# Performance work log

Hardware: AMD Instinct MI355X
Metric: run time of the kernel (lower is better)

## Reference

```python
import jax, jax.numpy as jnp
import numpy as np
from jax import lax

FEAT_STRIDE = 16
BOX_SIZES = (4.0, 8.0, 12.0, 16.0, 24.0, 32.0, 48.0, 64.0, 96.0)
SCALE = 1.0
NUM_ANCHORS = 9
MIN_SIZE = 3.0          # rpn_config.MIN_SIZE (feature-map units)
NMS_THRESH = 0.7        # rpn_config.NMS_THRESH
PRE_NMS_TOP_N = 6000    # rpn_config.PRE_NMS_TOP_N
POST_NMS_TOP_N = 300    # rpn_config.POST_NMS_TOP_N


def _generate_anchors(H, W):
    # [A,H,W,4] boxes in (x, y, w, h); coord 0 pairs with the height axis,
    # matching clip_boxes_batch which clips index 0/2 against `length`=height.
    s = jnp.asarray(BOX_SIZES, jnp.float32) * SCALE                  # [A]
    cy = jnp.arange(H, dtype=jnp.float32) + 0.5
    cx = jnp.arange(W, dtype=jnp.float32) + 0.5
    shp = (NUM_ANCHORS, H, W)
    x0 = jnp.broadcast_to(cy[None, :, None] - s[:, None, None] / 2, shp)
    y0 = jnp.broadcast_to(cx[None, None, :] - s[:, None, None] / 2, shp)
    wh = jnp.broadcast_to(s[:, None, None], shp)
    return jnp.stack([x0, y0, wh, wh], axis=-1)


def _clip_boxes(boxes, H, W):
    # Faithful to clip_boxes_batch: clamp all entries at 0, convert to corners,
    # clamp x against height, y against width, convert back to (x,y,w,h).
    b = jnp.maximum(boxes, 0.0)
    x1, y1, w, h = b[..., 0], b[..., 1], b[..., 2], b[..., 3]
    x2, y2 = x1 + w, y1 + h
    x1 = jnp.minimum(x1, H)
    y1 = jnp.minimum(y1, W)
    x2 = jnp.minimum(x2, H)
    y2 = jnp.minimum(y2, W)
    return jnp.stack([x1, y1, x2 - x1, y2 - y1], axis=-1)


def setup_inputs() -> dict:
    key = jax.random.key(0)
    k1, k2 = jax.random.split(key)
    scores = jax.random.uniform(k1, (1, NUM_ANCHORS, 128, 128), dtype=jnp.float32)
    bbox_deltas = jax.random.normal(k2, (1, 4 * NUM_ANCHORS, 128, 128), dtype=jnp.float32)
    image_metadata = jnp.zeros((1, 3), dtype=jnp.float32)  # unused by forward
    return {"scores": scores, "bbox_deltas": bbox_deltas, "image_metadata": image_metadata}


def reference(scores, bbox_deltas, image_metadata):
    b, A, H, W = scores.shape
    anchors = _generate_anchors(H, W)[None]                 # [1,A,H,W,4]
    # torch view chain (A*4,H,W)->(A,4,H,W)->(A,H,W,4) over contiguous memory
    # is a single reshape of the flat buffer:
    deltas = bbox_deltas.reshape(b, A, H, W, 4)
    boxes = _clip_boxes(anchors + deltas, float(H), float(W))
    flat = boxes.reshape(-1, 4)                             # [N,4], N=A*H*W
    keep = (flat[:, 2] >= MIN_SIZE) & (flat[:, 3] >= MIN_SIZE)
    sc = jnp.where(keep, scores.reshape(-1), -jnp.inf)      # mask instead of compaction (jit-safe)
    _, top = lax.top_k(sc, PRE_NMS_TOP_N)                   # score-descending pre-NMS top-N
    props = flat[top]                                       # [K,4]

    # --- greedy NMS, processing order = descending y2 (as in source `nms`) ---
    x1, y1, w, h = props[:, 0], props[:, 1], props[:, 2], props[:, 3]
    x2, y2 = x1 + w, y1 + h
    order = jnp.argsort(-y2)
    x1, y1, x2, y2 = x1[order], y1[order], x2[order], y2[order]
    area = jnp.maximum((x2 - x1) * (y2 - y1), 1e-6)         # areas = l*b in source
    iw = jnp.maximum(jnp.minimum(x2[:, None], x2[None, :]) - jnp.maximum(x1[:, None], x1[None, :]) + 1.0, 0.0)
    ih = jnp.maximum(jnp.minimum(y2[:, None], y2[None, :]) - jnp.maximum(y1[:, None], y1[None, :]) + 1.0, 0.0)
    ov = iw * ih / area[None, :]                            # intersection / area[j], as in source

    K = PRE_NMS_TOP_N

    def body(valid, i):
        supp = (ov[i] >= NMS_THRESH) & valid
        supp = supp.at[i].set(False)
        return jnp.where(valid[i], valid & ~supp, valid), None

    valid, _ = lax.scan(body, jnp.ones((K,), bool), jnp.arange(K))

    # kept boxes first, in processing order; pad with zeros to POST_NMS_TOP_N
    perm = jnp.argsort(jnp.where(valid, jnp.arange(K), K))
    sel = perm[:POST_NMS_TOP_N]
    out = props[order][sel] * valid[sel][:, None].astype(props.dtype)
    return out[None]                                        # [1, POST_NMS_TOP_N, 4]
```

## Files before the change

kernel.cpp:

```cpp
#include <hip/hip_runtime.h>
#include <cstdint>
#include <cstddef>

#define N_TOT   147456
#define K_PRE   6000
#define K_POST  300
#define CAP     32768
#define MW      188
#define ROWS_PAD 6144
#define CH      256
#define NCH     24
#define CT      128
#define ROWB    24
#define COLB    47
#define NTILE   (ROWB*COLB)
#define G       16
#define NBLK    576
#define HBLK    144
#define NGRP    24
#define GSZ     24

#define OFF_CAND 0u
#define OFF_P    262144u
#define OFF_YK   358144u
#define OFF_OP   406272u
#define OFF_Q    502272u
#define OFF_BND  598272u
#define OFF_MASK 622336u

__constant__ float c_sizes[9] = {4.f,8.f,12.f,16.f,24.f,32.f,48.f,64.f,96.f};

__device__ uint32_t g_hist[4096];
__device__ uint32_t g_cnt;
__device__ uint32_t g_barL[8][NGRP * 16];
__device__ uint32_t g_barR[8 * 16];
__device__ uint32_t g_rel[8][NGRP * 16];

__device__ __forceinline__ void astore32(uint32_t* p, uint32_t v) {
    __hip_atomic_store(p, v, __ATOMIC_RELAXED, __HIP_MEMORY_SCOPE_AGENT);
}
__device__ __forceinline__ void astore64(uint64_t* p, uint64_t v) {
    __hip_atomic_store(p, v, __ATOMIC_RELAXED, __HIP_MEMORY_SCOPE_AGENT);
}
__device__ __forceinline__ void astoreF4(float4* p, float4 v) {
    union { float4 f; uint64_t u[2]; } c; c.f = v;
    astore64((uint64_t*)p, c.u[0]);
    astore64(((uint64_t*)p) + 1, c.u[1]);
}

__device__ __forceinline__ void flagBarrier(int i) {
    __syncthreads();
    if (threadIdx.x == 0) {
        int grp = (int)(blockIdx.x / GSZ);
        int mem = (int)(blockIdx.x % GSZ);
        uint32_t t = __hip_atomic_fetch_add(&g_barL[i][grp * 16], 1u,
                          __ATOMIC_RELAXED, __HIP_MEMORY_SCOPE_AGENT);
        uint32_t round = t / GSZ;
        if ((t % GSZ) == GSZ - 1u)
            __hip_atomic_fetch_add(&g_barR[i * 16], 1u,
                __ATOMIC_RELAXED, __HIP_MEMORY_SCOPE_AGENT);
        uint32_t tries = 0;
        if (mem == 0) {
            uint32_t target = (round + 1u) * NGRP;
            while (__hip_atomic_load(&g_barR[i * 16], __ATOMIC_RELAXED,
                                     __HIP_MEMORY_SCOPE_AGENT) < target) {
                __builtin_amdgcn_s_sleep(4);
                if (++tries > (1u << 20)) break;
            }
            astore32(&g_rel[i][grp * 16], round + 1u);
        } else {
            while (__hip_atomic_load(&g_rel[i][grp * 16], __ATOMIC_RELAXED,
                                     __HIP_MEMORY_SCOPE_AGENT) < round + 1u) {
                __builtin_amdgcn_s_sleep(4);
                if (++tries > (1u << 20)) break;
            }
        }
        asm volatile("" ::: "memory");
    }
    __syncthreads();
}

__device__ __forceinline__ void compute_box(int idx, const float* __restrict__ deltas,
                                            float& px1, float& py1, float& pw, float& ph) {
    int a   = idx >> 14;
    int rem = idx & 16383;
    int h   = rem >> 7;
    int w   = rem & 127;
    float s    = c_sizes[a];
    float half = s * 0.5f;
    const float4 d = *(const float4*)(deltas + (size_t)a * 65536 + (size_t)rem * 4);
    float b0 = (((float)h + 0.5f) - half) + d.x;
    float b1 = (((float)w + 0.5f) - half) + d.y;
    float b2 = s + d.z;
    float b3 = s + d.w;
    b0 = fmaxf(b0, 0.0f); b1 = fmaxf(b1, 0.0f);
    b2 = fmaxf(b2, 0.0f); b3 = fmaxf(b3, 0.0f);
    float x1 = b0, y1 = b1;
    float x2 = b0 + b2, y2 = b1 + b3;
    x1 = fminf(x1, 128.0f); y1 = fminf(y1, 128.0f);
    x2 = fminf(x2, 128.0f); y2 = fminf(y2, 128.0f);
    px1 = x1; py1 = y1; pw = x2 - x1; ph = y2 - y1;
}

__device__ __forceinline__ uint32_t waveReduceSum(uint32_t v) {
    #pragma unroll
    for (int o = 32; o > 0; o >>= 1) v += __shfl_xor(v, o, 64);
    return v;
}

__global__ void __launch_bounds__(256, 4) mega(const float* __restrict__ scores,
                                               const float* __restrict__ deltas,
                                               float* __restrict__ out,
                                               char* __restrict__ ws) {
    __shared__ __align__(16) char smem[17664];

    uint64_t* cand = (uint64_t*)(ws + OFF_CAND);
    float4*   P    = (float4*)(ws + OFF_P);
    uint64_t* yk   = (uint64_t*)(ws + OFF_YK);
    float4*   OP   = (float4*)(ws + OFF_OP);
    float4*   Q    = (float4*)(ws + OFF_Q);
    float*    Bnd  = (float*)(ws + OFF_BND);
    uint32_t* mask = (uint32_t*)(ws + OFF_MASK);

    const int tid  = threadIdx.x;
    const int bid  = blockIdx.x;
    const int wave = tid >> 6, lane = tid & 63;

    uint32_t k4x = 0, k4y = 0, k4z = 0, k4w = 0;

    if (bid < HBLK) {
        uint32_t* lh = (uint32_t*)smem;
        for (int i = tid; i < 4096; i += 256) lh[i] = 0u;
        __syncthreads();
        int t4 = (bid * 256 + tid) * 4;
        float4 sc4 = *(const float4*)(scores + t4);
        uint32_t k4[4];
        #pragma unroll
        for (int e = 0; e < 4; e++) {
            int idx = t4 + e;
            float px1, py1, pw, ph;
            compute_box(idx, deltas, px1, py1, pw, ph);
            bool keep = (pw >= 3.0f) && (ph >= 3.0f);
            float sc = (&sc4.x)[e];
            uint32_t key = keep ? __float_as_uint(sc) : 0u;
            k4[e] = key;
            atomicAdd(&lh[key >> 20], 1u);
        }
        k4x = k4[0]; k4y = k4[1]; k4z = k4[2]; k4w = k4[3];
        __syncthreads();
        for (int i = tid; i < 4096; i += 256) {
            uint32_t v = lh[i];
            if (v) atomicAdd(&g_hist[i], v);
        }
    }
    flagBarrier(0);

    if (bid < HBLK) {
        uint32_t* lh   = (uint32_t*)smem;
        uint32_t* seg  = (uint32_t*)(smem + 16384);
        uint32_t* bshp = (uint32_t*)(smem + 16384 + 1024);
        uint32_t* lcnt = bshp + 1;
        uint32_t* lbas = bshp + 2;
        if (tid == 0) lcnt[0] = 0u;
        for (int i = tid; i < 4096; i += 256) lh[i] = g_hist[i];
        __syncthreads();
        uint32_t s = 0;
        #pragma unroll
        for (int q = 0; q < 16; q++) s += lh[tid * 16 + q];
        seg[tid] = s;
        __syncthreads();
        for (int off = 1; off < 256; off <<= 1) {
            uint32_t v = seg[tid];
            if (tid + off < 256) v += seg[tid + off];
            __syncthreads();
            seg[tid] = v;
            __syncthreads();
        }
        uint32_t St  = seg[tid];
        uint32_t St1 = (tid < 255) ? seg[tid + 1] : 0u;
        if (St >= K_PRE && St1 < K_PRE) {
            uint32_t c2 = St1;
            uint32_t bstar = 0u;
            for (int q = 15; q >= 0; q--) {
                c2 += lh[tid * 16 + q];
                if (c2 >= K_PRE) { bstar = (uint32_t)(tid * 16 + q); break; }
            }
            bshp[0] = bstar;
        }
        if (tid == 0 && seg[0] < K_PRE) bshp[0] = 0u;
        __syncthreads();
        uint32_t bstar = bshp[0];
        int t4 = (bid * 256 + tid) * 4;
        bool s0 = (k4x >> 20) >= bstar;
        bool s1 = (k4y >> 20) >= bstar;
        bool s2 = (k4z >> 20) >= bstar;
        bool s3 = (k4w >> 20) >= bstar;
        uint32_t nsel = (uint32_t)s0 + s1 + s2 + s3;
        uint32_t myoff = 0u;
        if (nsel) myoff = atomicAdd(lcnt, nsel);
        __syncthreads();
        if (tid == 0) lbas[0] = atomicAdd(&g_cnt, lcnt[0]);
        __syncthreads();
        uint32_t pos = lbas[0] + myoff;
        if (s0) { if (pos < CAP) astore64(&cand[pos], ((uint64_t)k4x << 32) | (uint32_t)(~(uint32_t)(t4 + 0))); pos++; }
        if (s1) { if (pos < CAP) astore64(&cand[pos], ((uint64_t)k4y << 32) | (uint32_t)(~(uint32_t)(t4 + 1))); pos++; }
        if (s2) { if (pos < CAP) astore64(&cand[pos], ((uint64_t)k4z << 32) | (uint32_t)(~(uint32_t)(t4 + 2))); pos++; }
        if (s3) { if (pos < CAP) astore64(&cand[pos], ((uint64_t)k4w << 32) | (uint32_t)(~(uint32_t)(t4 + 3))); }
    }
    flagBarrier(1);

    {
        uint32_t (*part)[G] = (uint32_t (*)[G])smem;
        uint32_t C = g_cnt;
        if (C > CAP) C = CAP;
        uint32_t nGroups = (C + G - 1) / G;
        for (uint32_t g = bid; g < nGroups; g += NBLK) {
            uint32_t b = g * G;
            uint64_t m[G];
            uint32_t cnt[G];
            #pragma unroll
            for (int q = 0; q < G; q++) {
                m[q] = (b + q < C) ? cand[b + q] : ~0ull;
                cnt[q] = 0u;
            }
            for (uint32_t j0 = 0; j0 < C; j0 += 1024) {
                uint32_t ja = j0 + tid, jb = ja + 256, jc = ja + 512, jd = ja + 768;
                uint64_t ka = (ja < C) ? cand[ja] : 0ull;
                uint64_t kb = (jb < C) ? cand[jb] : 0ull;
                uint64_t kc = (jc < C) ? cand[jc] : 0ull;
                uint64_t kd = (jd < C) ? cand[jd] : 0ull;
                #pragma unroll
                for (int q = 0; q < G; q++)
                    cnt[q] += (uint32_t)(ka > m[q]) + (uint32_t)(kb > m[q])
                            + (uint32_t)(kc > m[q]) + (uint32_t)(kd > m[q]);
            }
            #pragma unroll
            for (int q = 0; q < G; q++) cnt[q] = waveReduceSum(cnt[q]);
            if (lane == 0) {
                #pragma unroll
                for (int q = 0; q < G; q++) part[wave][q] = cnt[q];
            }
            __syncthreads();
            if (tid < G && b + tid < C) {
                uint32_t r = part[0][tid] + part[1][tid] + part[2][tid] + part[3][tid];
                if (r < K_PRE) {
                    int idx = (int)(~((uint32_t)cand[b + tid]));
                    float px1, py1, pw, ph;
                    compute_box(idx, deltas, px1, py1, pw, ph);
                    astoreF4(&P[r], make_float4(px1, py1, pw, ph));
                    float y2 = py1 + ph;
                    astore64(&yk[r], ((uint64_t)__float_as_uint(y2) << 32) | (uint32_t)(~r));
                }
            }
            __syncthreads();
        }
    }
    flagBarrier(2);

    if (bid < K_PRE / G) {
        uint32_t (*part)[G] = (uint32_t (*)[G])smem;
        uint32_t b = (uint32_t)bid * G;
        uint64_t m[G];
        uint32_t cnt[G];
        #pragma unroll
        for (int q = 0; q < G; q++) {
            m[q] = yk[b + q];
            cnt[q] = 0u;
        }
        for (uint32_t j0 = 0; j0 < K_PRE; j0 += 1024) {
            uint32_t ja = j0 + tid, jb = ja + 256, jc = ja + 512, jd = ja + 768;
            uint64_t ka = (ja < K_PRE) ? yk[ja] : 0ull;
            uint64_t kb = (jb < K_PRE) ? yk[jb] : 0ull;
            uint64_t kc = (jc < K_PRE) ? yk[jc] : 0ull;
            uint64_t kd = (jd < K_PRE) ? yk[jd] : 0ull;
            #pragma unroll
            for (int q = 0; q < G; q++)
                cnt[q] += (uint32_t)(ka > m[q]) + (uint32_t)(kb > m[q])
                        + (uint32_t)(kc > m[q]) + (uint32_t)(kd > m[q]);
        }
        #pragma unroll
        for (int q = 0; q < G; q++) cnt[q] = waveReduceSum(cnt[q]);
        if (lane == 0) {
            #pragma unroll
            for (int q = 0; q < G; q++) part[wave][q] = cnt[q];
        }
        __syncthreads();
        if (tid < G) {
            uint32_t r = part[0][tid] + part[1][tid] + part[2][tid] + part[3][tid];
            float4 p = P[b + tid];
            astoreF4(&OP[r], p);
            float x1 = p.x, y1 = p.y;
            float x2 = x1 + p.z, y2 = y1 + p.w;
            float area = fmaxf((x2 - x1) * (y2 - y1), 1e-6f);
            astoreF4(&Q[r], make_float4(x1, y1, x2, y2));
            const double Mc = (double)0.7f - 0x1.0p-25;
            double c = Mc * (double)area;
            float Bf = (float)c;
            if (!((double)Bf > c)) Bf = __int_as_float(__float_as_int(Bf) + 1);
            astore32((uint32_t*)&Bnd[r], __float_as_uint(Bf));
        }
    }
    flagBarrier(3);

    {
        float4* qs = (float4*)smem;
        float*  bs = (float*)(smem + CT * 16);
        for (uint32_t t = bid; t < NTILE; t += NBLK) {
            int bx = (int)(t % ROWB);
            int by = (int)(t / ROWB);
            int i  = bx * 256 + tid;
            int c0 = by * CT;
            int ncols = min(CT, K_PRE - c0);
            bool rowok = (i < K_PRE);
            float4 qi = rowok ? Q[i] : make_float4(0.f, 0.f, 0.f, 0.f);
            __syncthreads();
            for (int j = tid; j < ncols; j += 256) {
                qs[j] = Q[c0 + j];
                bs[j] = Bnd[c0 + j];
            }
            __syncthreads();
            uint32_t bw[4];
            #pragma unroll
            for (int w = 0; w < 4; w++) {
                uint32_t bits = 0u;
                int jb = w * 32;
                int jn = min(32, ncols - jb);
                #pragma unroll 8
                for (int b = 0; b < jn; b++) {
                    int j = jb + b;
                    float4 qj = qs[j];
                    float iw = fminf(qi.z, qj.z) - fmaxf(qi.x, qj.x) + 1.0f;
                    iw = fmaxf(iw, 0.0f);
                    float ih = fminf(qi.w, qj.w) - fmaxf(qi.y, qj.y) + 1.0f;
                    ih = fmaxf(ih, 0.0f);
                    float d = iw * ih;
                    bits |= (d >= bs[j]) ? (1u << b) : 0u;
                }
                int gj = c0 + jb;
                uint32_t selfo = (uint32_t)(i - gj);
                if (selfo < 32u) bits &= ~(1u << selfo);
                bw[w] = bits;
            }
            if (rowok) {
                uint64_t* bp = (uint64_t*)&mask[(size_t)i * MW + (c0 >> 5)];
                astore64(bp,     ((uint64_t)bw[1] << 32) | bw[0]);
                astore64(bp + 1, ((uint64_t)bw[3] << 32) | bw[2]);
            }
        }
    }
    flagBarrier(4);
    if (bid != 0) return;

    {
        uint32_t* rem  = (uint32_t*)smem;
        uint32_t* sidx = rem + 192;
        uint32_t* svL  = sidx + CH;
        uint32_t* pref = svL + 192;
        uint32_t* nsSh = pref + MW;
        if (tid < 16) {
            #pragma unroll
            for (int q = 0; q < 16; q++) g_hist[tid * 16 + q] = 0u;
        }
        if (tid == 16) g_cnt = 0u;
        if (tid < 192) { rem[tid] = 0u; svL[tid] = 0u; }
        for (int i = tid; i < K_POST * 4; i += 256) out[i] = 0.0f;
        __syncthreads();
        uint4 s00 = make_uint4(0,0,0,0), s01 = s00, s10 = s00, s11 = s00;
        uint4 s20 = s00, s21 = s00, s30 = s00, s31 = s00;
        if (tid < 64) {
            const uint32_t* p0 = mask + (size_t)(tid) * MW;
            s00 = *(const uint4*)p0;       s01 = *(const uint4*)(p0 + 4);
            const uint32_t* p1 = mask + (size_t)(64 + tid) * MW;
            s10 = *(const uint4*)p1;       s11 = *(const uint4*)(p1 + 4);
            const uint32_t* p2 = mask + (size_t)(128 + tid) * MW;
            s20 = *(const uint4*)p2;       s21 = *(const uint4*)(p2 + 4);
            const uint32_t* p3 = mask + (size_t)(192 + tid) * MW;
            s30 = *(const uint4*)p3;       s31 = *(const uint4*)(p3 + 4);
        }
        for (int c = 0; c < NCH; c++) {
            int base = c * CH;
            if (tid < 64) {
                uint64_t w0 = ~(((uint64_t)rem[8*c+1] << 32) | (uint64_t)rem[8*c+0]);
                uint64_t w1 = ~(((uint64_t)rem[8*c+3] << 32) | (uint64_t)rem[8*c+2]);
                uint64_t w2 = ~(((uint64_t)rem[8*c+5] << 32) | (uint64_t)rem[8*c+4]);
                uint64_t w3 = ~(((uint64_t)rem[8*c+7] << 32) | (uint64_t)rem[8*c+6]);
                int rows = K_PRE - base;
                if (rows < CH) {
                    auto msk = [](int v) -> uint64_t {
                        return v <= 0 ? 0ull : (v >= 64 ? ~0ull : ((1ull << v) - 1ull));
                    };
                    w0 &= msk(rows); w1 &= msk(rows - 64);
                    w2 &= msk(rows - 128); w3 &= msk(rows - 192);
                }
                uint64_t sv0 = 0ull, sv1 = 0ull, sv2 = 0ull, sv3 = 0ull;
                while (w0 | w1 | w2 | w3) {
                    int k;
                    uint32_t a0, a1, a2, a3, a4, a5, a6, a7;
                    if (w0) {
                        k = __ffsll((unsigned long long)w0) - 1;
                        sv0 |= 1ull << k; w0 &= ~(1ull << k);
                        a0 = (uint32_t)__builtin_amdgcn_readlane((int)s00.x, k);
                        a1 = (uint32_t)__builtin_amdgcn_readlane((int)s00.y, k);
                        a2 = (uint32_t)__builtin_amdgcn_readlane((int)s00.z, k);
                        a3 = (uint32_t)__builtin_amdgcn_readlane((int)s00.w, k);
                        a4 = (uint32_t)__builtin_amdgcn_readlane((int)s01.x, k);
                        a5 = (uint32_t)__builtin_amdgcn_readlane((int)s01.y, k);
                        a6 = (uint32_t)__builtin_amdgcn_readlane((int)s01.z, k);
                        a7 = (uint32_t)__builtin_amdgcn_readlane((int)s01.w, k);
                    } else if (w1) {
                        k = __ffsll((unsigned long long)w1) - 1;
                        sv1 |= 1ull << k; w1 &= ~(1ull << k);
                        a0 = (uint32_t)__builtin_amdgcn_readlane((int)s10.x, k);
                        a1 = (uint32_t)__builtin_amdgcn_readlane((int)s10.y, k);
                        a2 = (uint32_t)__builtin_amdgcn_readlane((int)s10.z, k);
                        a3 = (uint32_t)__builtin_amdgcn_readlane((int)s10.w, k);
                        a4 = (uint32_t)__builtin_amdgcn_readlane((int)s11.x, k);
                        a5 = (uint32_t)__builtin_amdgcn_readlane((int)s11.y, k);
                        a6 = (uint32_t)__builtin_amdgcn_readlane((int)s11.z, k);
                        a7 = (uint32_t)__builtin_amdgcn_readlane((int)s11.w, k);
                    } else if (w2) {
                        k = __ffsll((unsigned long long)w2) - 1;
                        sv2 |= 1ull << k; w2 &= ~(1ull << k);
                        a0 = (uint32_t)__builtin_amdgcn_readlane((int)s20.x, k);
                        a1 = (uint32_t)__builtin_amdgcn_readlane((int)s20.y, k);
                        a2 = (uint32_t)__builtin_amdgcn_readlane((int)s20.z, k);
                        a3 = (uint32_t)__builtin_amdgcn_readlane((int)s20.w, k);
                        a4 = (uint32_t)__builtin_amdgcn_readlane((int)s21.x, k);
                        a5 = (uint32_t)__builtin_amdgcn_readlane((int)s21.y, k);
                        a6 = (uint32_t)__builtin_amdgcn_readlane((int)s21.z, k);
                        a7 = (uint32_t)__builtin_amdgcn_readlane((int)s21.w, k);
                    } else {
                        k = __ffsll((unsigned long long)w3) - 1;
                        sv3 |= 1ull << k; w3 &= ~(1ull << k);
                        a0 = (uint32_t)__builtin_amdgcn_readlane((int)s30.x, k);
                        a1 = (uint32_t)__builtin_amdgcn_readlane((int)s30.y, k);
                        a2 = (uint32_t)__builtin_amdgcn_readlane((int)s30.z, k);
                        a3 = (uint32_t)__builtin_amdgcn_readlane((int)s30.w, k);
                        a4 = (uint32_t)__builtin_amdgcn_readlane((int)s31.x, k);
                        a5 = (uint32_t)__builtin_amdgcn_readlane((int)s31.y, k);
                        a6 = (uint32_t)__builtin_amdgcn_readlane((int)s31.z, k);
                        a7 = (uint32_t)__builtin_amdgcn_readlane((int)s31.w, k);
                    }
                    w0 &= ~(((uint64_t)a1 << 32) | (uint64_t)a0);
                    w1 &= ~(((uint64_t)a3 << 32) | (uint64_t)a2);
                    w2 &= ~(((uint64_t)a5 << 32) | (uint64_t)a4);
                    w3 &= ~(((uint64_t)a7 << 32) | (uint64_t)a6);
                }
                uint32_t n0 = (uint32_t)__popcll(sv0), n1 = (uint32_t)__popcll(sv1);
                uint32_t n2 = (uint32_t)__popcll(sv2), n3 = (uint32_t)__popcll(sv3);
                uint32_t o1 = n0, o2 = n0 + n1, o3 = n0 + n1 + n2, ns = o3 + n3;
                if (tid == 0) {
                    svL[8*c+0] = (uint32_t)sv0; svL[8*c+1] = (uint32_t)(sv0 >> 32);
                    svL[8*c+2] = (uint32_t)sv1; svL[8*c+3] = (uint32_t)(sv1 >> 32);
                    svL[8*c+4] = (uint32_t)sv2; svL[8*c+5] = (uint32_t)(sv2 >> 32);
                    svL[8*c+6] = (uint32_t)sv3; svL[8*c+7] = (uint32_t)(sv3 >> 32);
                    nsSh[0] = ns;
                }
                uint64_t lowm = (1ull << tid) - 1ull;
                if ((sv0 >> tid) & 1ull) sidx[      __popcll(sv0 & lowm)] = (uint32_t)(base + tid);
                if ((sv1 >> tid) & 1ull) sidx[o1 +  __popcll(sv1 & lowm)] = (uint32_t)(base + 64 + tid);
                if ((sv2 >> tid) & 1ull) sidx[o2 +  __popcll(sv2 & lowm)] = (uint32_t)(base + 128 + tid);
                if ((sv3 >> tid) & 1ull) sidx[o3 +  __popcll(sv3 & lowm)] = (uint32_t)(base + 192 + tid);
                if (ns) {
                    uint32_t nsPad = (ns + 31u) & ~31u;
                    uint32_t first;
                    if      (sv0) first = (uint32_t)base +       (uint32_t)(__ffsll((unsigned long long)sv0) - 1);
                    else if (sv1) first = (uint32_t)base + 64u + (uint32_t)(__ffsll((unsigned long long)sv1) - 1);
                    else if (sv2) first = (uint32_t)base + 128u+ (uint32_t)(__ffsll((unsigned long long)sv2) - 1);
                    else          first = (uint32_t)base + 192u+ (uint32_t)(__ffsll((unsigned long long)sv3) - 1);
                    #pragma unroll
                    for (int rr = 0; rr < 4; rr++) {
                        uint32_t ii = (uint32_t)tid + 64u * rr;
                        if (ii >= ns && ii < nsPad) sidx[ii] = first;
                    }
                }
                if (c + 1 < NCH) {
                    const uint32_t* p0 = mask + (size_t)(base + 256 + tid) * MW + 8*(c+1);
                    s00 = *(const uint4*)p0;  s01 = *(const uint4*)(p0 + 4);
                    const uint32_t* p1 = p0 + (size_t)64 * MW;
                    s10 = *(const uint4*)p1;  s11 = *(const uint4*)(p1 + 4);
                    const uint32_t* p2 = p1 + (size_t)64 * MW;
                    s20 = *(const uint4*)p2;  s21 = *(const uint4*)(p2 + 4);
                    const uint32_t* p3 = p2 + (size_t)64 * MW;
                    s30 = *(const uint4*)p3;  s31 = *(const uint4*)(p3 + 4);
                }
            }
            __syncthreads();
            int w = tid - 64;
            if (w >= 0 && w < MW) {
                uint32_t nsPad = (nsSh[0] + 31u) & ~31u;
                uint32_t acc = rem[w];
                for (uint32_t t2 = 0; t2 < nsPad; t2 += 32) {
                    uint32_t r[32];
                    #pragma unroll
                    for (int q = 0; q < 32; q++)
                        r[q] = mask[(size_t)sidx[t2 + q] * MW + w];
                    uint32_t o = 0u;
                    #pragma unroll
                    for (int q = 0; q < 32; q++) o |= r[q];
                    acc |= o;
                }
                rem[w] = acc;
            }
            __syncthreads();
        }
        if (tid < MW) {
            uint32_t vv = svL[tid] & ~rem[tid];
            if (tid == MW - 1) vv &= 0xFFFFu;
            rem[tid] = vv;
        }
        __syncthreads();
        if (tid == 0) {
            uint32_t run = 0;
            for (int w2 = 0; w2 < MW; w2++) { pref[w2] = run; run += (uint32_t)__popc(rem[w2]); }
        }
        __syncthreads();
        if (tid < MW) {
            uint32_t b = rem[tid];
            uint32_t r = pref[tid];
            int basebit = tid * 32;
            while (b && r < K_POST) {
                int bit = __ffs(b) - 1;
                b &= b - 1u;
                float4 pp = OP[basebit + bit];
                *(float4*)(out + (size_t)r * 4) = pp;
                r++;
            }
        }
    }
}

extern "C" void kernel_launch(void* const* d_in, const int* in_sizes, int n_in,
                              void* d_out, int out_size, void* d_ws, size_t ws_size,
                              hipStream_t stream) {
    (void)in_sizes; (void)n_in; (void)out_size; (void)ws_size;
    const float* scores = (const float*)d_in[0];
    const float* deltas = (const float*)d_in[1];
    float* out = (float*)d_out;
    char* ws = (char*)d_ws;
    mega<<<NBLK, 256, 0, stream>>>(scores, deltas, out, ws);
}
```

Measured before the change: 159.4 us.

## Split final NMS scan into separate kernel and scope first barrier to histogram blocks

The last grid barrier is replaced by a kernel boundary: the mask-building kernel ends and a separate single-block kernel runs the greedy NMS scan and output compaction. The first barrier now synchronizes only the 144 histogram blocks, so the other blocks skip it. The barrier sleep interval is halved, and some atomic stores become plain stores now that kernel-boundary ordering applies. This trades one spin barrier across all blocks for an extra launch gap.

New measurement: 154.9 us. 1.03x faster.

```diff
diff --git a/kernel.cpp b/kernel.cpp
--- a/kernel.cpp
+++ b/kernel.cpp
@@ -17,7 +17,6 @@
 #define G       16
 #define NBLK    576
 #define HBLK    144
-#define NGRP    24
 #define GSZ     24
 
 #define OFF_CAND 0u
@@ -32,9 +31,9 @@
 
 __device__ uint32_t g_hist[4096];
 __device__ uint32_t g_cnt;
-__device__ uint32_t g_barL[8][NGRP * 16];
-__device__ uint32_t g_barR[8 * 16];
-__device__ uint32_t g_rel[8][NGRP * 16];
+__device__ uint32_t g_barL[4][GSZ * 16];
+__device__ uint32_t g_barR[4 * 16];
+__device__ uint32_t g_rel[4][GSZ * 16];
 
 __device__ __forceinline__ void astore32(uint32_t* p, uint32_t v) {
     __hip_atomic_store(p, v, __ATOMIC_RELAXED, __HIP_MEMORY_SCOPE_AGENT);
@@ -48,11 +47,12 @@
     astore64(((uint64_t*)p) + 1, c.u[1]);
 }
 
-__device__ __forceinline__ void flagBarrier(int i) {
+__device__ __forceinline__ void treeBarrier(int i, int nprt) {
     __syncthreads();
     if (threadIdx.x == 0) {
-        int grp = (int)(blockIdx.x / GSZ);
-        int mem = (int)(blockIdx.x % GSZ);
+        int ngrp = nprt / GSZ;
+        int grp  = (int)(blockIdx.x / GSZ);
+        int mem  = (int)(blockIdx.x % GSZ);
         uint32_t t = __hip_atomic_fetch_add(&g_barL[i][grp * 16], 1u,
                           __ATOMIC_RELAXED, __HIP_MEMORY_SCOPE_AGENT);
         uint32_t round = t / GSZ;
@@ -61,17 +61,17 @@
                 __ATOMIC_RELAXED, __HIP_MEMORY_SCOPE_AGENT);
         uint32_t tries = 0;
         if (mem == 0) {
-            uint32_t target = (round + 1u) * NGRP;
+            uint32_t target = (round + 1u) * (uint32_t)ngrp;
             while (__hip_atomic_load(&g_barR[i * 16], __ATOMIC_RELAXED,
                                      __HIP_MEMORY_SCOPE_AGENT) < target) {
-                __builtin_amdgcn_s_sleep(4);
+                __builtin_amdgcn_s_sleep(2);
                 if (++tries > (1u << 20)) break;
             }
             astore32(&g_rel[i][grp * 16], round + 1u);
         } else {
             while (__hip_atomic_load(&g_rel[i][grp * 16], __ATOMIC_RELAXED,
                                      __HIP_MEMORY_SCOPE_AGENT) < round + 1u) {
-                __builtin_amdgcn_s_sleep(4);
+                __builtin_amdgcn_s_sleep(2);
                 if (++tries > (1u << 20)) break;
             }
         }
@@ -108,10 +108,9 @@
     return v;
 }
 
-__global__ void __launch_bounds__(256, 4) mega(const float* __restrict__ scores,
-                                               const float* __restrict__ deltas,
-                                               float* __restrict__ out,
-                                               char* __restrict__ ws) {
+__global__ void __launch_bounds__(256, 4) fusedA(const float* __restrict__ scores,
+                                                 const float* __restrict__ deltas,
+                                                 char* __restrict__ ws) {
     __shared__ __align__(16) char smem[17664];
 
     uint64_t* cand = (uint64_t*)(ws + OFF_CAND);
@@ -126,88 +125,88 @@
     const int bid  = blockIdx.x;
     const int wave = tid >> 6, lane = tid & 63;
 
-    uint32_t k4x = 0, k4y = 0, k4z = 0, k4w = 0;
-
     if (bid < HBLK) {
-        uint32_t* lh = (uint32_t*)smem;
-        for (int i = tid; i < 4096; i += 256) lh[i] = 0u;
-        __syncthreads();
-        int t4 = (bid * 256 + tid) * 4;
-        float4 sc4 = *(const float4*)(scores + t4);
-        uint32_t k4[4];
-        #pragma unroll
-        for (int e = 0; e < 4; e++) {
-            int idx = t4 + e;
-            float px1, py1, pw, ph;
-            compute_box(idx, deltas, px1, py1, pw, ph);
-            bool keep = (pw >= 3.0f) && (ph >= 3.0f);
-            float sc = (&sc4.x)[e];
-            uint32_t key = keep ? __float_as_uint(sc) : 0u;
-            k4[e] = key;
-            atomicAdd(&lh[key >> 20], 1u);
-        }
-        k4x = k4[0]; k4y = k4[1]; k4z = k4[2]; k4w = k4[3];
-        __syncthreads();
-        for (int i = tid; i < 4096; i += 256) {
-            uint32_t v = lh[i];
-            if (v) atomicAdd(&g_hist[i], v);
-        }
-    }
-    flagBarrier(0);
-
-    if (bid < HBLK) {
-        uint32_t* lh   = (uint32_t*)smem;
-        uint32_t* seg  = (uint32_t*)(smem + 16384);
-        uint32_t* bshp = (uint32_t*)(smem + 16384 + 1024);
-        uint32_t* lcnt = bshp + 1;
-        uint32_t* lbas = bshp + 2;
-        if (tid == 0) lcnt[0] = 0u;
-        for (int i = tid; i < 4096; i += 256) lh[i] = g_hist[i];
-        __syncthreads();
-        uint32_t s = 0;
-        #pragma unroll
-        for (int q = 0; q < 16; q++) s += lh[tid * 16 + q];
-        seg[tid] = s;
-        __syncthreads();
-        for (int off = 1; off < 256; off <<= 1) {
-            uint32_t v = seg[tid];
-            if (tid + off < 256) v += seg[tid + off];
-            __syncthreads();
-            seg[tid] = v;
-            __syncthreads();
-        }
-        uint32_t St  = seg[tid];
-        uint32_t St1 = (tid < 255) ? seg[tid + 1] : 0u;
-        if (St >= K_PRE && St1 < K_PRE) {
-            uint32_t c2 = St1;
-            uint32_t bstar = 0u;
-            for (int q = 15; q >= 0; q--) {
-                c2 += lh[tid * 16 + q];
-                if (c2 >= K_PRE) { bstar = (uint32_t)(tid * 16 + q); break; }
-            }
-            bshp[0] = bstar;
-        }
-        if (tid == 0 && seg[0] < K_PRE) bshp[0] = 0u;
-        __syncthreads();
-        uint32_t bstar = bshp[0];
-        int t4 = (bid * 256 + tid) * 4;
-        bool s0 = (k4x >> 20) >= bstar;
-        bool s1 = (k4y >> 20) >= bstar;
-        bool s2 = (k4z >> 20) >= bstar;
-        bool s3 = (k4w >> 20) >= bstar;
-        uint32_t nsel = (uint32_t)s0 + s1 + s2 + s3;
-        uint32_t myoff = 0u;
-        if (nsel) myoff = atomicAdd(lcnt, nsel);
-        __syncthreads();
-        if (tid == 0) lbas[0] = atomicAdd(&g_cnt, lcnt[0]);
-        __syncthreads();
-        uint32_t pos = lbas[0] + myoff;
-        if (s0) { if (pos < CAP) astore64(&cand[pos], ((uint64_t)k4x << 32) | (uint32_t)(~(uint32_t)(t4 + 0))); pos++; }
-        if (s1) { if (pos < CAP) astore64(&cand[pos], ((uint64_t)k4y << 32) | (uint32_t)(~(uint32_t)(t4 + 1))); pos++; }
-        if (s2) { if (pos < CAP) astore64(&cand[pos], ((uint64_t)k4z << 32) | (uint32_t)(~(uint32_t)(t4 + 2))); pos++; }
-        if (s3) { if (pos < CAP) astore64(&cand[pos], ((uint64_t)k4w << 32) | (uint32_t)(~(uint32_t)(t4 + 3))); }
-    }
-    flagBarrier(1);
+        uint32_t k4x, k4y, k4z, k4w;
+        {
+            uint32_t* lh = (uint32_t*)smem;
+            for (int i = tid; i < 4096; i += 256) lh[i] = 0u;
+            __syncthreads();
+            int t4 = (bid * 256 + tid) * 4;
+            float4 sc4 = *(const float4*)(scores + t4);
+            uint32_t k4[4];
+            #pragma unroll
+            for (int e = 0; e < 4; e++) {
+                int idx = t4 + e;
+                float px1, py1, pw, ph;
+                compute_box(idx, deltas, px1, py1, pw, ph);
+                bool keep = (pw >= 3.0f) && (ph >= 3.0f);
+                float sc = (&sc4.x)[e];
+                uint32_t key = keep ? __float_as_uint(sc) : 0u;
+                k4[e] = key;
+                atomicAdd(&lh[key >> 20], 1u);
+            }
+            k4x = k4[0]; k4y = k4[1]; k4z = k4[2]; k4w = k4[3];
+            __syncthreads();
+            for (int i = tid; i < 4096; i += 256) {
+                uint32_t v = lh[i];
+                if (v) atomicAdd(&g_hist[i], v);
+            }
+        }
+        treeBarrier(0, HBLK);
+        {
+            uint32_t* lh   = (uint32_t*)smem;
+            uint32_t* seg  = (uint32_t*)(smem + 16384);
+            uint32_t* bshp = (uint32_t*)(smem + 16384 + 1024);
+            uint32_t* lcnt = bshp + 1;
+            uint32_t* lbas = bshp + 2;
+            if (tid == 0) lcnt[0] = 0u;
+            for (int i = tid; i < 4096; i += 256) lh[i] = g_hist[i];
+            __syncthreads();
+            uint32_t s = 0;
+            #pragma unroll
+            for (int q = 0; q < 16; q++) s += lh[tid * 16 + q];
+            seg[tid] = s;
+            __syncthreads();
+            for (int off = 1; off < 256; off <<= 1) {
+                uint32_t v = seg[tid];
+                if (tid + off < 256) v += seg[tid + off];
+                __syncthreads();
+                seg[tid] = v;
+                __syncthreads();
+            }
+            uint32_t St  = seg[tid];
+            uint32_t St1 = (tid < 255) ? seg[tid + 1] : 0u;
+            if (St >= K_PRE && St1 < K_PRE) {
+                uint32_t c2 = St1;
+                uint32_t bstar = 0u;
+                for (int q = 15; q >= 0; q--) {
+                    c2 += lh[tid * 16 + q];
+                    if (c2 >= K_PRE) { bstar = (uint32_t)(tid * 16 + q); break; }
+                }
+                bshp[0] = bstar;
+            }
+            if (tid == 0 && seg[0] < K_PRE) bshp[0] = 0u;
+            __syncthreads();
+            uint32_t bstar = bshp[0];
+            int t4 = (bid * 256 + tid) * 4;
+            bool s0 = (k4x >> 20) >= bstar;
+            bool s1 = (k4y >> 20) >= bstar;
+            bool s2 = (k4z >> 20) >= bstar;
+            bool s3 = (k4w >> 20) >= bstar;
+            uint32_t nsel = (uint32_t)s0 + s1 + s2 + s3;
+            uint32_t myoff = 0u;
+            if (nsel) myoff = atomicAdd(lcnt, nsel);
+            __syncthreads();
+            if (tid == 0) lbas[0] = atomicAdd(&g_cnt, lcnt[0]);
+            __syncthreads();
+            uint32_t pos = lbas[0] + myoff;
+            if (s0) { if (pos < CAP) astore64(&cand[pos], ((uint64_t)k4x << 32) | (uint32_t)(~(uint32_t)(t4 + 0))); pos++; }
+            if (s1) { if (pos < CAP) astore64(&cand[pos], ((uint64_t)k4y << 32) | (uint32_t)(~(uint32_t)(t4 + 1))); pos++; }
+            if (s2) { if (pos < CAP) astore64(&cand[pos], ((uint64_t)k4z << 32) | (uint32_t)(~(uint32_t)(t4 + 2))); pos++; }
+            if (s3) { if (pos < CAP) astore64(&cand[pos], ((uint64_t)k4w << 32) | (uint32_t)(~(uint32_t)(t4 + 3))); }
+        }
+    }
+    treeBarrier(1, NBLK);
 
     {
         uint32_t (*part)[G] = (uint32_t (*)[G])smem;
@@ -255,7 +254,7 @@
             __syncthreads();
         }
     }
-    flagBarrier(2);
+    treeBarrier(2, NBLK);
 
     if (bid < K_PRE / G) {
         uint32_t (*part)[G] = (uint32_t (*)[G])smem;
@@ -288,7 +287,7 @@
         if (tid < G) {
             uint32_t r = part[0][tid] + part[1][tid] + part[2][tid] + part[3][tid];
             float4 p = P[b + tid];
-            astoreF4(&OP[r], p);
+            OP[r] = p;
             float x1 = p.x, y1 = p.y;
             float x2 = x1 + p.z, y2 = y1 + p.w;
             float area = fmaxf((x2 - x1) * (y2 - y1), 1e-6f);
@@ -300,7 +299,7 @@
             astore32((uint32_t*)&Bnd[r], __float_as_uint(Bf));
         }
     }
-    flagBarrier(3);
+    treeBarrier(3, NBLK);
 
     {
         float4* qs = (float4*)smem;
@@ -342,190 +341,190 @@
                 bw[w] = bits;
             }
             if (rowok) {
-                uint64_t* bp = (uint64_t*)&mask[(size_t)i * MW + (c0 >> 5)];
-                astore64(bp,     ((uint64_t)bw[1] << 32) | bw[0]);
-                astore64(bp + 1, ((uint64_t)bw[3] << 32) | bw[2]);
-            }
-        }
-    }
-    flagBarrier(4);
-    if (bid != 0) return;
-
-    {
-        uint32_t* rem  = (uint32_t*)smem;
-        uint32_t* sidx = rem + 192;
-        uint32_t* svL  = sidx + CH;
-        uint32_t* pref = svL + 192;
-        uint32_t* nsSh = pref + MW;
-        if (tid < 16) {
-            #pragma unroll
-            for (int q = 0; q < 16; q++) g_hist[tid * 16 + q] = 0u;
-        }
-        if (tid == 16) g_cnt = 0u;
-        if (tid < 192) { rem[tid] = 0u; svL[tid] = 0u; }
-        for (int i = tid; i < K_POST * 4; i += 256) out[i] = 0.0f;
+                *(uint4*)&mask[(size_t)i * MW + (c0 >> 5)] =
+                    make_uint4(bw[0], bw[1], bw[2], bw[3]);
+            }
+        }
+    }
+}
+
+__global__ void __launch_bounds__(256) k_scan(const uint32_t* __restrict__ mask,
+                                              const float4* __restrict__ OP,
+                                              float* __restrict__ out) {
+    __shared__ uint32_t rem[192];
+    __shared__ uint32_t sidx[CH];
+    __shared__ uint32_t svL[192];
+    __shared__ uint32_t nsSh;
+    __shared__ uint32_t pref[MW];
+    int tid = threadIdx.x;
+    if (tid < 16) {
+        #pragma unroll
+        for (int q = 0; q < 16; q++) g_hist[tid * 16 + q] = 0u;
+    }
+    if (tid == 16) g_cnt = 0u;
+    if (tid < 192) { rem[tid] = 0u; svL[tid] = 0u; }
+    for (int i = tid; i < K_POST * 4; i += 256) out[i] = 0.0f;
+    __syncthreads();
+    uint4 s00 = make_uint4(0,0,0,0), s01 = s00, s10 = s00, s11 = s00;
+    uint4 s20 = s00, s21 = s00, s30 = s00, s31 = s00;
+    if (tid < 64) {
+        const uint32_t* p0 = mask + (size_t)(tid) * MW;
+        s00 = *(const uint4*)p0;       s01 = *(const uint4*)(p0 + 4);
+        const uint32_t* p1 = mask + (size_t)(64 + tid) * MW;
+        s10 = *(const uint4*)p1;       s11 = *(const uint4*)(p1 + 4);
+        const uint32_t* p2 = mask + (size_t)(128 + tid) * MW;
+        s20 = *(const uint4*)p2;       s21 = *(const uint4*)(p2 + 4);
+        const uint32_t* p3 = mask + (size_t)(192 + tid) * MW;
+        s30 = *(const uint4*)p3;       s31 = *(const uint4*)(p3 + 4);
+    }
+    for (int c = 0; c < NCH; c++) {
+        int base = c * CH;
+        if (tid < 64) {
+            uint64_t w0 = ~(((uint64_t)rem[8*c+1] << 32) | (uint64_t)rem[8*c+0]);
+            uint64_t w1 = ~(((uint64_t)rem[8*c+3] << 32) | (uint64_t)rem[8*c+2]);
+            uint64_t w2 = ~(((uint64_t)rem[8*c+5] << 32) | (uint64_t)rem[8*c+4]);
+            uint64_t w3 = ~(((uint64_t)rem[8*c+7] << 32) | (uint64_t)rem[8*c+6]);
+            int rows = K_PRE - base;
+            if (rows < CH) {
+                auto msk = [](int v) -> uint64_t {
+                    return v <= 0 ? 0ull : (v >= 64 ? ~0ull : ((1ull << v) - 1ull));
+                };
+                w0 &= msk(rows); w1 &= msk(rows - 64);
+                w2 &= msk(rows - 128); w3 &= msk(rows - 192);
+            }
+            uint64_t sv0 = 0ull, sv1 = 0ull, sv2 = 0ull, sv3 = 0ull;
+            while (w0 | w1 | w2 | w3) {
+                int k;
+                uint32_t a0, a1, a2, a3, a4, a5, a6, a7;
+                if (w0) {
+                    k = __ffsll((unsigned long long)w0) - 1;
+                    sv0 |= 1ull << k; w0 &= ~(1ull << k);
+                    a0 = (uint32_t)__builtin_amdgcn_readlane((int)s00.x, k);
+                    a1 = (uint32_t)__builtin_amdgcn_readlane((int)s00.y, k);
+                    a2 = (uint32_t)__builtin_amdgcn_readlane((int)s00.z, k);
+                    a3 = (uint32_t)__builtin_amdgcn_readlane((int)s00.w, k);
+                    a4 = (uint32_t)__builtin_amdgcn_readlane((int)s01.x, k);
+                    a5 = (uint32_t)__builtin_amdgcn_readlane((int)s01.y, k);
+                    a6 = (uint32_t)__builtin_amdgcn_readlane((int)s01.z, k);
+                    a7 = (uint32_t)__builtin_amdgcn_readlane((int)s01.w, k);
+                } else if (w1) {
+                    k = __ffsll((unsigned long long)w1) - 1;
+                    sv1 |= 1ull << k; w1 &= ~(1ull << k);
+                    a0 = (uint32_t)__builtin_amdgcn_readlane((int)s10.x, k);
+                    a1 = (uint32_t)__builtin_amdgcn_readlane((int)s10.y, k);
+                    a2 = (uint32_t)__builtin_amdgcn_readlane((int)s10.z, k);
+                    a3 = (uint32_t)__builtin_amdgcn_readlane((int)s10.w, k);
+                    a4 = (uint32_t)__builtin_amdgcn_readlane((int)s11.x, k);
+                    a5 = (uint32_t)__builtin_amdgcn_readlane((int)s11.y, k);
+                    a6 = (uint32_t)__builtin_amdgcn_readlane((int)s11.z, k);
+                    a7 = (uint32_t)__builtin_amdgcn_readlane((int)s11.w, k);
+                } else if (w2) {
+                    k = __ffsll((unsigned long long)w2) - 1;
+                    sv2 |= 1ull << k; w2 &= ~(1ull << k);
+                    a0 = (uint32_t)__builtin_amdgcn_readlane((int)s20.x, k);
+                    a1 = (uint32_t)__builtin_amdgcn_readlane((int)s20.y, k);
+                    a2 = (uint32_t)__builtin_amdgcn_readlane((int)s20.z, k);
+                    a3 = (uint32_t)__builtin_amdgcn_readlane((int)s20.w, k);
+                    a4 = (uint32_t)__builtin_amdgcn_readlane((int)s21.x, k);
+                    a5 = (uint32_t)__builtin_amdgcn_readlane((int)s21.y, k);
+                    a6 = (uint32_t)__builtin_amdgcn_readlane((int)s21.z, k);
+                    a7 = (uint32_t)__builtin_amdgcn_readlane((int)s21.w, k);
+                } else {
+                    k = __ffsll((unsigned long long)w3) - 1;
+                    sv3 |= 1ull << k; w3 &= ~(1ull << k);
+                    a0 = (uint32_t)__builtin_amdgcn_readlane((int)s30.x, k);
+                    a1 = (uint32_t)__builtin_amdgcn_readlane((int)s30.y, k);
+                    a2 = (uint32_t)__builtin_amdgcn_readlane((int)s30.z, k);
+                    a3 = (uint32_t)__builtin_amdgcn_readlane((int)s30.w, k);
+                    a4 = (uint32_t)__builtin_amdgcn_readlane((int)s31.x, k);
+                    a5 = (uint32_t)__builtin_amdgcn_readlane((int)s31.y, k);
+                    a6 = (uint32_t)__builtin_amdgcn_readlane((int)s31.z, k);
+                    a7 = (uint32_t)__builtin_amdgcn_readlane((int)s31.w, k);
+                }
+                w0 &= ~(((uint64_t)a1 << 32) | (uint64_t)a0);
+                w1 &= ~(((uint64_t)a3 << 32) | (uint64_t)a2);
+                w2 &= ~(((uint64_t)a5 << 32) | (uint64_t)a4);
+                w3 &= ~(((uint64_t)a7 << 32) | (uint64_t)a6);
+            }
+            uint32_t n0 = (uint32_t)__popcll(sv0), n1 = (uint32_t)__popcll(sv1);
+            uint32_t n2 = (uint32_t)__popcll(sv2), n3 = (uint32_t)__popcll(sv3);
+            uint32_t o1 = n0, o2 = n0 + n1, o3 = n0 + n1 + n2, ns = o3 + n3;
+            if (tid == 0) {
+                svL[8*c+0] = (uint32_t)sv0; svL[8*c+1] = (uint32_t)(sv0 >> 32);
+                svL[8*c+2] = (uint32_t)sv1; svL[8*c+3] = (uint32_t)(sv1 >> 32);
+                svL[8*c+4] = (uint32_t)sv2; svL[8*c+5] = (uint32_t)(sv2 >> 32);
+                svL[8*c+6] = (uint32_t)sv3; svL[8*c+7] = (uint32_t)(sv3 >> 32);
+                nsSh = ns;
+            }
+            uint64_t lowm = (1ull << tid) - 1ull;
+            if ((sv0 >> tid) & 1ull) sidx[      __popcll(sv0 & lowm)] = (uint32_t)(base + tid);
+            if ((sv1 >> tid) & 1ull) sidx[o1 +  __popcll(sv1 & lowm)] = (uint32_t)(base + 64 + tid);
+            if ((sv2 >> tid) & 1ull) sidx[o2 +  __popcll(sv2 & lowm)] = (uint32_t)(base + 128 + tid);
+            if ((sv3 >> tid) & 1ull) sidx[o3 +  __popcll(sv3 & lowm)] = (uint32_t)(base + 192 + tid);
+            if (ns) {
+                uint32_t nsPad = (ns + 31u) & ~31u;
+                uint32_t first;
+                if      (sv0) first = (uint32_t)base +       (uint32_t)(__ffsll((unsigned long long)sv0) - 1);
+                else if (sv1) first = (uint32_t)base + 64u + (uint32_t)(__ffsll((unsigned long long)sv1) - 1);
+                else if (sv2) first = (uint32_t)base + 128u+ (uint32_t)(__ffsll((unsigned long long)sv2) - 1);
+                else          first = (uint32_t)base + 192u+ (uint32_t)(__ffsll((unsigned long long)sv3) - 1);
+                #pragma unroll
+                for (int rr = 0; rr < 4; rr++) {
+                    uint32_t ii = (uint32_t)tid + 64u * rr;
+                    if (ii >= ns && ii < nsPad) sidx[ii] = first;
+                }
+            }
+            if (c + 1 < NCH) {
+                const uint32_t* p0 = mask + (size_t)(base + 256 + tid) * MW + 8*(c+1);
+                s00 = *(const uint4*)p0;  s01 = *(const uint4*)(p0 + 4);
+                const uint32_t* p1 = p0 + (size_t)64 * MW;
+                s10 = *(const uint4*)p1;  s11 = *(const uint4*)(p1 + 4);
+                const uint32_t* p2 = p1 + (size_t)64 * MW;
+                s20 = *(const uint4*)p2;  s21 = *(const uint4*)(p2 + 4);
+                const uint32_t* p3 = p2 + (size_t)64 * MW;
+                s30 = *(const uint4*)p3;  s31 = *(const uint4*)(p3 + 4);
+            }
+        }
         __syncthreads();
-        uint4 s00 = make_uint4(0,0,0,0), s01 = s00, s10 = s00, s11 = s00;
-        uint4 s20 = s00, s21 = s00, s30 = s00, s31 = s00;
-        if (tid < 64) {
-            const uint32_t* p0 = mask + (size_t)(tid) * MW;
-            s00 = *(const uint4*)p0;       s01 = *(const uint4*)(p0 + 4);
-            const uint32_t* p1 = mask + (size_t)(64 + tid) * MW;
-            s10 = *(const uint4*)p1;       s11 = *(const uint4*)(p1 + 4);
-            const uint32_t* p2 = mask + (size_t)(128 + tid) * MW;
-            s20 = *(const uint4*)p2;       s21 = *(const uint4*)(p2 + 4);
-            const uint32_t* p3 = mask + (size_t)(192 + tid) * MW;
-            s30 = *(const uint4*)p3;       s31 = *(const uint4*)(p3 + 4);
-        }
-        for (int c = 0; c < NCH; c++) {
-            int base = c * CH;
-            if (tid < 64) {
-                uint64_t w0 = ~(((uint64_t)rem[8*c+1] << 32) | (uint64_t)rem[8*c+0]);
-                uint64_t w1 = ~(((uint64_t)rem[8*c+3] << 32) | (uint64_t)rem[8*c+2]);
-                uint64_t w2 = ~(((uint64_t)rem[8*c+5] << 32) | (uint64_t)rem[8*c+4]);
-                uint64_t w3 = ~(((uint64_t)rem[8*c+7] << 32) | (uint64_t)rem[8*c+6]);
-                int rows = K_PRE - base;
-                if (rows < CH) {
-                    auto msk = [](int v) -> uint64_t {
-                        return v <= 0 ? 0ull : (v >= 64 ? ~0ull : ((1ull << v) - 1ull));
-                    };
-                    w0 &= msk(rows); w1 &= msk(rows - 64);
-                    w2 &= msk(rows - 128); w3 &= msk(rows - 192);
-                }
-                uint64_t sv0 = 0ull, sv1 = 0ull, sv2 = 0ull, sv3 = 0ull;
-                while (w0 | w1 | w2 | w3) {
-                    int k;
-                    uint32_t a0, a1, a2, a3, a4, a5, a6, a7;
-                    if (w0) {
-                        k = __ffsll((unsigned long long)w0) - 1;
-                        sv0 |= 1ull << k; w0 &= ~(1ull << k);
-                        a0 = (uint32_t)__builtin_amdgcn_readlane((int)s00.x, k);
-                        a1 = (uint32_t)__builtin_amdgcn_readlane((int)s00.y, k);
-                        a2 = (uint32_t)__builtin_amdgcn_readlane((int)s00.z, k);
-                        a3 = (uint32_t)__builtin_amdgcn_readlane((int)s00.w, k);
-                        a4 = (uint32_t)__builtin_amdgcn_readlane((int)s01.x, k);
-                        a5 = (uint32_t)__builtin_amdgcn_readlane((int)s01.y, k);
-                        a6 = (uint32_t)__builtin_amdgcn_readlane((int)s01.z, k);
-                        a7 = (uint32_t)__builtin_amdgcn_readlane((int)s01.w, k);
-                    } else if (w1) {
-                        k = __ffsll((unsigned long long)w1) - 1;
-                        sv1 |= 1ull << k; w1 &= ~(1ull << k);
-                        a0 = (uint32_t)__builtin_amdgcn_readlane((int)s10.x, k);
-                        a1 = (uint32_t)__builtin_amdgcn_readlane((int)s10.y, k);
-                        a2 = (uint32_t)__builtin_amdgcn_readlane((int)s10.z, k);
-                        a3 = (uint32_t)__builtin_amdgcn_readlane((int)s10.w, k);
-                        a4 = (uint32_t)__builtin_amdgcn_readlane((int)s11.x, k);
-                        a5 = (uint32_t)__builtin_amdgcn_readlane((int)s11.y, k);
-                        a6 = (uint32_t)__builtin_amdgcn_readlane((int)s11.z, k);
-                        a7 = (uint32_t)__builtin_amdgcn_readlane((int)s11.w, k);
-                    } else if (w2) {
-                        k = __ffsll((unsigned long long)w2) - 1;
-                        sv2 |= 1ull << k; w2 &= ~(1ull << k);
-                        a0 = (uint32_t)__builtin_amdgcn_readlane((int)s20.x, k);
-                        a1 = (uint32_t)__builtin_amdgcn_readlane((int)s20.y, k);
-                        a2 = (uint32_t)__builtin_amdgcn_readlane((int)s20.z, k);
-                        a3 = (uint32_t)__builtin_amdgcn_readlane((int)s20.w, k);
-                        a4 = (uint32_t)__builtin_amdgcn_readlane((int)s21.x, k);
-                        a5 = (uint32_t)__builtin_amdgcn_readlane((int)s21.y, k);
-                        a6 = (uint32_t)__builtin_amdgcn_readlane((int)s21.z, k);
-                        a7 = (uint32_t)__builtin_amdgcn_readlane((int)s21.w, k);
-                    } else {
-                        k = __ffsll((unsigned long long)w3) - 1;
-                        sv3 |= 1ull << k; w3 &= ~(1ull << k);
-                        a0 = (uint32_t)__builtin_amdgcn_readlane((int)s30.x, k);
-                        a1 = (uint32_t)__builtin_amdgcn_readlane((int)s30.y, k);
-                        a2 = (uint32_t)__builtin_amdgcn_readlane((int)s30.z, k);
-                        a3 = (uint32_t)__builtin_amdgcn_readlane((int)s30.w, k);
-                        a4 = (uint32_t)__builtin_amdgcn_readlane((int)s31.x, k);
-                        a5 = (uint32_t)__builtin_amdgcn_readlane((int)s31.y, k);
-                        a6 = (uint32_t)__builtin_amdgcn_readlane((int)s31.z, k);
-                        a7 = (uint32_t)__builtin_amdgcn_readlane((int)s31.w, k);
-                    }
-                    w0 &= ~(((uint64_t)a1 << 32) | (uint64_t)a0);
-                    w1 &= ~(((uint64_t)a3 << 32) | (uint64_t)a2);
-                    w2 &= ~(((uint64_t)a5 << 32) | (uint64_t)a4);
-                    w3 &= ~(((uint64_t)a7 << 32) | (uint64_t)a6);
-                }
-                uint32_t n0 = (uint32_t)__popcll(sv0), n1 = (uint32_t)__popcll(sv1);
-                uint32_t n2 = (uint32_t)__popcll(sv2), n3 = (uint32_t)__popcll(sv3);
-                uint32_t o1 = n0, o2 = n0 + n1, o3 = n0 + n1 + n2, ns = o3 + n3;
-                if (tid == 0) {
-                    svL[8*c+0] = (uint32_t)sv0; svL[8*c+1] = (uint32_t)(sv0 >> 32);
-                    svL[8*c+2] = (uint32_t)sv1; svL[8*c+3] = (uint32_t)(sv1 >> 32);
-                    svL[8*c+4] = (uint32_t)sv2; svL[8*c+5] = (uint32_t)(sv2 >> 32);
-                    svL[8*c+6] = (uint32_t)sv3; svL[8*c+7] = (uint32_t)(sv3 >> 32);
-                    nsSh[0] = ns;
-                }
-                uint64_t lowm = (1ull << tid) - 1ull;
-                if ((sv0 >> tid) & 1ull) sidx[      __popcll(sv0 & lowm)] = (uint32_t)(base + tid);
-                if ((sv1 >> tid) & 1ull) sidx[o1 +  __popcll(sv1 & lowm)] = (uint32_t)(base + 64 + tid);
-                if ((sv2 >> tid) & 1ull) sidx[o2 +  __popcll(sv2 & lowm)] = (uint32_t)(base + 128 + tid);
-                if ((sv3 >> tid) & 1ull) sidx[o3 +  __popcll(sv3 & lowm)] = (uint32_t)(base + 192 + tid);
-                if (ns) {
-                    uint32_t nsPad = (ns + 31u) & ~31u;
-                    uint32_t first;
-                    if      (sv0) first = (uint32_t)base +       (uint32_t)(__ffsll((unsigned long long)sv0) - 1);
-                    else if (sv1) first = (uint32_t)base + 64u + (uint32_t)(__ffsll((unsigned long long)sv1) - 1);
-                    else if (sv2) first = (uint32_t)base + 128u+ (uint32_t)(__ffsll((unsigned long long)sv2) - 1);
-                    else          first = (uint32_t)base + 192u+ (uint32_t)(__ffsll((unsigned long long)sv3) - 1);
-                    #pragma unroll
-                    for (int rr = 0; rr < 4; rr++) {
-                        uint32_t ii = (uint32_t)tid + 64u * rr;
-                        if (ii >= ns && ii < nsPad) sidx[ii] = first;
-                    }
-                }
-                if (c + 1 < NCH) {
-                    const uint32_t* p0 = mask + (size_t)(base + 256 + tid) * MW + 8*(c+1);
-                    s00 = *(const uint4*)p0;  s01 = *(const uint4*)(p0 + 4);
-                    const uint32_t* p1 = p0 + (size_t)64 * MW;
-                    s10 = *(const uint4*)p1;  s11 = *(const uint4*)(p1 + 4);
-                    const uint32_t* p2 = p1 + (size_t)64 * MW;
-                    s20 = *(const uint4*)p2;  s21 = *(const uint4*)(p2 + 4);
-                    const uint32_t* p3 = p2 + (size_t)64 * MW;
-                    s30 = *(const uint4*)p3;  s31 = *(const uint4*)(p3 + 4);
-                }
-            }
-            __syncthreads();
-            int w = tid - 64;
-            if (w >= 0 && w < MW) {
-                uint32_t nsPad = (nsSh[0] + 31u) & ~31u;
-                uint32_t acc = rem[w];
-                for (uint32_t t2 = 0; t2 < nsPad; t2 += 32) {
-                    uint32_t r[32];
-                    #pragma unroll
-                    for (int q = 0; q < 32; q++)
-                        r[q] = mask[(size_t)sidx[t2 + q] * MW + w];
-                    uint32_t o = 0u;
-                    #pragma unroll
-                    for (int q = 0; q < 32; q++) o |= r[q];
-                    acc |= o;
-                }
-                rem[w] = acc;
-            }
-            __syncthreads();
-        }
-        if (tid < MW) {
-            uint32_t vv = svL[tid] & ~rem[tid];
-            if (tid == MW - 1) vv &= 0xFFFFu;
-            rem[tid] = vv;
+        int w = tid - 64;
+        if (w >= 0 && w < MW) {
+            uint32_t nsPad = (nsSh + 31u) & ~31u;
+            uint32_t acc = rem[w];
+            for (uint32_t t2 = 0; t2 < nsPad; t2 += 32) {
+                uint32_t r[32];
+                #pragma unroll
+                for (int q = 0; q < 32; q++)
+                    r[q] = mask[(size_t)sidx[t2 + q] * MW + w];
+                uint32_t o = 0u;
+                #pragma unroll
+                for (int q = 0; q < 32; q++) o |= r[q];
+                acc |= o;
+            }
+            rem[w] = acc;
         }
         __syncthreads();
-        if (tid == 0) {
-            uint32_t run = 0;
-            for (int w2 = 0; w2 < MW; w2++) { pref[w2] = run; run += (uint32_t)__popc(rem[w2]); }
-        }
-        __syncthreads();
-        if (tid < MW) {
-            uint32_t b = rem[tid];
-            uint32_t r = pref[tid];
-            int basebit = tid * 32;
-            while (b && r < K_POST) {
-                int bit = __ffs(b) - 1;
-                b &= b - 1u;
-                float4 pp = OP[basebit + bit];
-                *(float4*)(out + (size_t)r * 4) = pp;
-                r++;
-            }
+    }
+    if (tid < MW) {
+        uint32_t vv = svL[tid] & ~rem[tid];
+        if (tid == MW - 1) vv &= 0xFFFFu;
+        rem[tid] = vv;
+    }
+    __syncthreads();
+    if (tid == 0) {
+        uint32_t run = 0;
+        for (int w2 = 0; w2 < MW; w2++) { pref[w2] = run; run += (uint32_t)__popc(rem[w2]); }
+    }
+    __syncthreads();
+    if (tid < MW) {
+        uint32_t b = rem[tid];
+        uint32_t r = pref[tid];
+        int basebit = tid * 32;
+        while (b && r < K_POST) {
+            int bit = __ffs(b) - 1;
+            b &= b - 1u;
+            float4 pp = OP[basebit + bit];
+            *(float4*)(out + (size_t)r * 4) = pp;
+            r++;
         }
     }
 }
@@ -538,5 +537,7 @@
     const float* deltas = (const float*)d_in[1];
     float* out = (float*)d_out;
     char* ws = (char*)d_ws;
-    mega<<<NBLK, 256, 0, stream>>>(scores, deltas, out, ws);
-}
+    fusedA<<<NBLK, 256, 0, stream>>>(scores, deltas, ws);
+    k_scan<<<1, 256, 0, stream>>>((const uint32_t*)(ws + OFF_MASK),
+                                  (const float4*)(ws + OFF_OP), out);
+}
```
